# Kernel optimization log

Measured on AMD Instinct MI355X. Metric: run time of the kernel, lower is better.

Reference implementation:

```python
import jax, jax.numpy as jnp
import numpy as np

B, T, C = 4, 2048, 1024
H, D = 16, 64  # num_heads, head_size; H*D == C


def setup_inputs() -> dict:
    key = jax.random.key(0)
    ks = jax.random.split(key, 6)
    s = C ** -0.5
    return {
        "x": jax.random.normal(ks[0], (B, T, C), dtype=jnp.float32),
        "Wq": jax.random.normal(ks[1], (H, C, D), dtype=jnp.float32) * s,
        "Wk": jax.random.normal(ks[2], (H, C, D), dtype=jnp.float32) * s,
        "Wv": jax.random.normal(ks[3], (H, C, D), dtype=jnp.float32) * s,
        "Wo": jax.random.normal(ks[4], (C, C), dtype=jnp.float32) * s,
        "bo": jnp.zeros((C,), dtype=jnp.float32),
    }


def reference(x, Wq, Wk, Wv, Wo, bo):
    # Per-head projections, vectorized over heads: [B,T,C] x [H,C,D] -> [B,H,T,D]
    q = jnp.einsum("btc,hcd->bhtd", x, Wq)
    k = jnp.einsum("btc,hcd->bhtd", x, Wk)
    v = jnp.einsum("btc,hcd->bhtd", x, Wv)
    # NOTE: original scales by n_embd**-0.5 (input channel C), not head_size.
    scale = jnp.asarray(C, x.dtype) ** -0.5
    scores = jnp.einsum("bhtd,bhsd->bhts", q, k) * scale  # [B,H,T,T]
    causal = jnp.tril(jnp.ones((T, T), dtype=bool))
    scores = jnp.where(causal, scores, jnp.asarray(-jnp.inf, x.dtype))
    attn = jax.nn.softmax(scores, axis=-1)
    out = jnp.einsum("bhts,bhsd->bhtd", attn, v)  # [B,H,T,D]
    # concat heads: [B,T,H*D] == [B,T,C]
    out = out.transpose(0, 2, 1, 3).reshape(B, T, H * D)
    return out @ Wo.T + bo
```

## Files before the change

kernel.cpp:

```cpp
#include <hip/hip_runtime.h>
#include <hip/hip_bf16.h>
#include <math.h>

#define B_ 4
#define T_ 2048
#define C_ 1024
#define H_ 16
#define D_ 64
#define BT (B_*T_)
#define BH (B_*H_)

typedef __bf16 bf16x8 __attribute__((ext_vector_type(8)));
typedef __bf16 bf16x4 __attribute__((ext_vector_type(4)));
typedef float f32x4 __attribute__((ext_vector_type(4)));
typedef unsigned short u16;
typedef u16 u16x8 __attribute__((ext_vector_type(8)));

#define GLL(g, l) __builtin_amdgcn_global_load_lds( \
    (const __attribute__((address_space(1))) unsigned int*)(g), \
    (__attribute__((address_space(3))) unsigned int*)(l), 16, 0, 0)

#define SCALE2 0.04508422f

__device__ __forceinline__ u16 f2b(float f) {
    union { float f; unsigned u; } v; v.f = f;
    unsigned r = v.u + 0x7fffu + ((v.u >> 16) & 1u);
    return (u16)(r >> 16);
}

__global__ __launch_bounds__(256) void prep(const float* __restrict__ x,
                                            const float* __restrict__ Wo,
                                            const float* __restrict__ Wq,
                                            const float* __restrict__ Wk,
                                            const float* __restrict__ Wv,
                                            u16* __restrict__ xbf,
                                            u16* __restrict__ wobf,
                                            u16* __restrict__ wt) {
    __shared__ u16 lds[64][72];
    int bid = blockIdx.x, tid = threadIdx.x;
    if (bid < 8192) {
        int g = bid * 256 + tid;
        float4 v = ((const float4*)x)[g];
        ushort4 o;
        o.x = f2b(v.x); o.y = f2b(v.y); o.z = f2b(v.z); o.w = f2b(v.w);
        ((ushort4*)xbf)[g] = o;
        return;
    }
    if (bid < 9216) {
        int g = (bid - 8192) * 256 + tid;
        float4 v = ((const float4*)Wo)[g];
        ushort4 o;
        o.x = f2b(v.x); o.y = f2b(v.y); o.z = f2b(v.z); o.w = f2b(v.w);
        ((ushort4*)wobf)[g] = o;
        return;
    }
    int id = bid - 9216;
    int cb = id & 15, h = (id >> 4) & 15, w = id >> 8;
    const float* W = (w == 0) ? Wq : (w == 1) ? Wk : Wv;
    float sc = (w == 0) ? SCALE2 : 1.0f;
    int c0 = cb * 64;
    {
        int col = (tid & 15) * 4;
        for (int cc = 0; cc < 4; ++cc) {
            int r = (tid >> 4) + cc * 16;
            float4 v = *(const float4*)&W[(size_t)(h * C_ + c0 + r) * D_ + col];
            lds[r][col + 0] = f2b(v.x * sc); lds[r][col + 1] = f2b(v.y * sc);
            lds[r][col + 2] = f2b(v.z * sc); lds[r][col + 3] = f2b(v.w * sc);
        }
    }
    __syncthreads();
    {
        int tcol = (tid & 7) * 8;
        for (int cc = 0; cc < 2; ++cc) {
            int d = (tid >> 3) + cc * 32;
            u16x8 t;
            for (int j = 0; j < 8; ++j) t[j] = lds[tcol + j][d];
            *(u16x8*)&wt[(((size_t)(w * H_ + h) * D_ + d) * C_) + c0 + tcol] = t;
        }
    }
}

__global__ __launch_bounds__(256) void qkv_gemm(const u16* __restrict__ xbf,
                                                const u16* __restrict__ wt,
                                                u16* __restrict__ q, u16* __restrict__ k,
                                                u16* __restrict__ vt) {
    __shared__ u16 Al[128][64];
    __shared__ u16 Bl[128][64];
    int mb = blockIdx.x, nb = blockIdx.y;
    int tid = threadIdx.x, wv = tid >> 6, lane = tid & 63, l15 = lane & 15, quad = lane >> 4;
    int rowh = (wv & 1) * 64, colh = (wv >> 1) * 64;
    f32x4 acc[4][4];
    #pragma unroll
    for (int i = 0; i < 4; ++i)
        #pragma unroll
        for (int j = 0; j < 4; ++j) acc[i][j] = (f32x4){0.f, 0.f, 0.f, 0.f};
    int lrow = lane >> 3;
    int srow = wv * 32 + lrow;
    int scol = (((lane & 7) ^ lrow)) * 8;
    const u16* agp = &xbf[(size_t)(mb * 128 + srow) * C_ + scol];
    const u16* bgp = &wt[(size_t)(nb * 128 + srow) * C_ + scol];
    int rsw = l15 & 7;
    for (int k0 = 0; k0 < C_; k0 += 64) {
        #pragma unroll
        for (int j = 0; j < 4; ++j) {
            GLL(agp + (size_t)(j * 8) * C_ + k0, &Al[wv * 32 + j * 8][0]);
            GLL(bgp + (size_t)(j * 8) * C_ + k0, &Bl[wv * 32 + j * 8][0]);
        }
        __syncthreads();
        #pragma unroll
        for (int ks = 0; ks < 2; ++ks) {
            int cbl = (((ks << 2) | quad) ^ rsw) * 8;
            bf16x8 af[4], bf[4];
            #pragma unroll
            for (int mt = 0; mt < 4; ++mt)
                af[mt] = *(const bf16x8*)&Al[rowh + mt * 16 + l15][cbl];
            #pragma unroll
            for (int nt = 0; nt < 4; ++nt)
                bf[nt] = *(const bf16x8*)&Bl[colh + nt * 16 + l15][cbl];
            #pragma unroll
            for (int mt = 0; mt < 4; ++mt)
                #pragma unroll
                for (int nt = 0; nt < 4; ++nt)
                    acc[mt][nt] = __builtin_amdgcn_mfma_f32_16x16x32_bf16(af[mt], bf[nt], acc[mt][nt], 0, 0, 0);
        }
        __syncthreads();
    }
    int bb = (mb * 128) >> 11;
    #pragma unroll
    for (int nt = 0; nt < 4; ++nt) {
        int n0 = nb * 128 + colh + nt * 16;
        int wsel = n0 >> 10, hh = (n0 >> 6) & 15, d0 = n0 & 63;
        if (wsel == 2) {
            u16* vrow = vt + ((size_t)((bb * H_ + hh) * D_) + d0 + l15) * T_;
            #pragma unroll
            for (int mt = 0; mt < 4; ++mt) {
                int tbase = ((mb * 128 + rowh + mt * 16) & (T_ - 1)) + quad * 4;
                bf16x4 w;
                #pragma unroll
                for (int r = 0; r < 4; ++r) w[r] = (__bf16)acc[mt][nt][r];
                *(bf16x4*)&vrow[tbase] = w;
            }
        } else {
            u16* op = (wsel == 0) ? q : k;
            #pragma unroll
            for (int mt = 0; mt < 4; ++mt)
                #pragma unroll
                for (int r = 0; r < 4; ++r) {
                    int m = mb * 128 + rowh + mt * 16 + quad * 4 + r;
                    int tt = m & (T_ - 1);
                    op[((size_t)(bb * H_ + hh) * T_ + tt) * D_ + d0 + l15] = f2b(acc[mt][nt][r]);
                }
        }
    }
}

__global__ __launch_bounds__(256, 2) void attn(const u16* __restrict__ q, const u16* __restrict__ kk,
                                               const u16* __restrict__ vt, u16* __restrict__ att) {
    __shared__ u16 Kl[2][64][64];
    __shared__ u16 Vl[2][64][64];
    __shared__ u16 Pl[4][32][72];
    int bh = blockIdx.x, c = 15 - blockIdx.y;
    int b = bh >> 4, h = bh & 15;
    int tid = threadIdx.x, wid = tid >> 6, lane = tid & 63, l15 = lane & 15, quad = lane >> 4;
    const u16* qbase = q + (size_t)bh * T_ * D_;
    const u16* kbase = kk + (size_t)bh * T_ * D_;
    const u16* vbase = vt + (size_t)bh * D_ * T_;
    u16* pw = &Pl[wid][0][0];
    bf16x8 ones;
    #pragma unroll
    for (int j = 0; j < 8; ++j) ones[j] = (__bf16)1.0f;
    int r8 = lane >> 3, cbl_st = lane & 7;
    int csrc = ((cbl_st ^ r8)) * 8;
    int strow = wid * 16 + r8;
    int rsw = l15 & 7;

    int R0q = c * 128 + wid * 32;
    int ktb = 2 * c + 1;
    int kmax_w = R0q >> 6;
    bf16x8 bq[2][2];
    #pragma unroll
    for (int qt = 0; qt < 2; ++qt)
        #pragma unroll
        for (int kd = 0; kd < 2; ++kd)
            bq[qt][kd] = *(const bf16x8*)&qbase[(size_t)(R0q + qt * 16 + l15) * D_ + kd * 32 + quad * 8];
    f32x4 o[4][2];
    f32x4 lacc[2];
    #pragma unroll
    for (int dt = 0; dt < 4; ++dt)
        #pragma unroll
        for (int qt = 0; qt < 2; ++qt) o[dt][qt] = (f32x4){0.f, 0.f, 0.f, 0.f};
    lacc[0] = (f32x4){0.f, 0.f, 0.f, 0.f};
    lacc[1] = (f32x4){0.f, 0.f, 0.f, 0.f};
    #pragma unroll
    for (int j = 0; j < 2; ++j) {
        GLL(kbase + (size_t)(strow + j * 8) * D_ + csrc, &Kl[0][wid * 16 + j * 8][0]);
        GLL(vbase + (size_t)(strow + j * 8) * T_ + csrc, &Vl[0][wid * 16 + j * 8][0]);
    }
    __syncthreads();
    for (int kt = 0; kt <= ktb; ++kt) {
        int cur = kt & 1;
        if (kt < ktb) {
            int kn = (kt + 1) * 64;
            #pragma unroll
            for (int j = 0; j < 2; ++j) {
                GLL(kbase + (size_t)(kn + strow + j * 8) * D_ + csrc, &Kl[cur ^ 1][wid * 16 + j * 8][0]);
                GLL(vbase + (size_t)(strow + j * 8) * T_ + kn + csrc, &Vl[cur ^ 1][wid * 16 + j * 8][0]);
            }
        }
        if (kt <= kmax_w) {
            int k0 = kt * 64;
            f32x4 sS[4][2];
            #pragma unroll
            for (int kvt = 0; kvt < 4; ++kvt)
                #pragma unroll
                for (int qt = 0; qt < 2; ++qt) sS[kvt][qt] = (f32x4){0.f, 0.f, 0.f, 0.f};
            #pragma unroll
            for (int kd = 0; kd < 2; ++kd) {
                int cblk = (((kd << 2) | quad) ^ rsw) * 8;
                bf16x8 akf[4];
                #pragma unroll
                for (int kvt = 0; kvt < 4; ++kvt)
                    akf[kvt] = *(const bf16x8*)&Kl[cur][kvt * 16 + l15][cblk];
                #pragma unroll
                for (int kvt = 0; kvt < 4; ++kvt)
                    #pragma unroll
                    for (int qt = 0; qt < 2; ++qt)
                        sS[kvt][qt] = __builtin_amdgcn_mfma_f32_16x16x32_bf16(akf[kvt], bq[qt][kd], sS[kvt][qt], 0, 0, 0);
            }
            if (kt == kmax_w) {
                #pragma unroll
                for (int qt = 0; qt < 2; ++qt) {
                    int qabs = R0q + qt * 16 + l15;
                    #pragma unroll
                    for (int kvt = 0; kvt < 4; ++kvt) {
                        int kvb = k0 + kvt * 16 + quad * 4;
                        #pragma unroll
                        for (int r = 0; r < 4; ++r)
                            if (kvb + r > qabs) sS[kvt][qt][r] = -INFINITY;
                    }
                }
            }
            #pragma unroll
            for (int kvt = 0; kvt < 4; ++kvt)
                #pragma unroll
                for (int qt = 0; qt < 2; ++qt)
                    #pragma unroll
                    for (int r = 0; r < 4; ++r)
                        sS[kvt][qt][r] = __builtin_amdgcn_exp2f(sS[kvt][qt][r]);
            #pragma unroll
            for (int qt = 0; qt < 2; ++qt)
                #pragma unroll
                for (int kvt = 0; kvt < 4; ++kvt) {
                    bf16x4 w;
                    #pragma unroll
                    for (int r = 0; r < 4; ++r) w[r] = (__bf16)sS[kvt][qt][r];
                    *(bf16x4*)&pw[(qt * 16 + l15) * 72 + kvt * 16 + quad * 4] = w;
                }
            #pragma unroll
            for (int ks = 0; ks < 2; ++ks) {
                int cblk = (((ks << 2) | quad) ^ rsw) * 8;
                bf16x8 avf[4];
                #pragma unroll
                for (int dt = 0; dt < 4; ++dt)
                    avf[dt] = *(const bf16x8*)&Vl[cur][dt * 16 + l15][cblk];
                #pragma unroll
                for (int qt = 0; qt < 2; ++qt) {
                    bf16x8 bp = *(const bf16x8*)&pw[(qt * 16 + l15) * 72 + ks * 32 + quad * 8];
                    #pragma unroll
                    for (int dt = 0; dt < 4; ++dt)
                        o[dt][qt] = __builtin_amdgcn_mfma_f32_16x16x32_bf16(avf[dt], bp, o[dt][qt], 0, 0, 0);
                    lacc[qt] = __builtin_amdgcn_mfma_f32_16x16x32_bf16(ones, bp, lacc[qt], 0, 0, 0);
                }
            }
        }
        __syncthreads();
    }
    #pragma unroll
    for (int qt = 0; qt < 2; ++qt) {
        float rl = __builtin_amdgcn_rcpf(lacc[qt][0]);
        int qabs = R0q + qt * 16 + l15;
        #pragma unroll
        for (int dt = 0; dt < 4; ++dt) {
            bf16x4 w;
            #pragma unroll
            for (int r = 0; r < 4; ++r) w[r] = (__bf16)(o[dt][qt][r] * rl);
            *(bf16x4*)&att[(size_t)(b * T_ + qabs) * C_ + h * 64 + dt * 16 + quad * 4] = w;
        }
    }
}

__global__ __launch_bounds__(256) void out_gemm(const u16* __restrict__ att,
                                                const u16* __restrict__ wo,
                                                const float* __restrict__ bo,
                                                float* __restrict__ out) {
    __shared__ u16 Al[128][64];
    __shared__ u16 Bl[128][64];
    int mb = blockIdx.x, nb = blockIdx.y;
    int tid = threadIdx.x, wv = tid >> 6, lane = tid & 63, l15 = lane & 15, quad = lane >> 4;
    int rowh = (wv & 1) * 64, colh = (wv >> 1) * 64;
    f32x4 acc[4][4];
    #pragma unroll
    for (int i = 0; i < 4; ++i)
        #pragma unroll
        for (int j = 0; j < 4; ++j) acc[i][j] = (f32x4){0.f, 0.f, 0.f, 0.f};
    int lrow = lane >> 3;
    int srow = wv * 32 + lrow;
    int scol = (((lane & 7) ^ lrow)) * 8;
    const u16* agp = &att[(size_t)(mb * 128 + srow) * C_ + scol];
    const u16* bgp = &wo[(size_t)(nb * 128 + srow) * C_ + scol];
    int rsw = l15 & 7;
    for (int k0 = 0; k0 < C_; k0 += 64) {
        #pragma unroll
        for (int j = 0; j < 4; ++j) {
            GLL(agp + (size_t)(j * 8) * C_ + k0, &Al[wv * 32 + j * 8][0]);
            GLL(bgp + (size_t)(j * 8) * C_ + k0, &Bl[wv * 32 + j * 8][0]);
        }
        __syncthreads();
        #pragma unroll
        for (int ks = 0; ks < 2; ++ks) {
            int cbl = (((ks << 2) | quad) ^ rsw) * 8;
            bf16x8 af[4], bf[4];
            #pragma unroll
            for (int mt = 0; mt < 4; ++mt)
                af[mt] = *(const bf16x8*)&Al[rowh + mt * 16 + l15][cbl];
            #pragma unroll
            for (int nt = 0; nt < 4; ++nt)
                bf[nt] = *(const bf16x8*)&Bl[colh + nt * 16 + l15][cbl];
            #pragma unroll
            for (int mt = 0; mt < 4; ++mt)
                #pragma unroll
                for (int nt = 0; nt < 4; ++nt)
                    acc[mt][nt] = __builtin_amdgcn_mfma_f32_16x16x32_bf16(af[mt], bf[nt], acc[mt][nt], 0, 0, 0);
        }
        __syncthreads();
    }
    #pragma unroll
    for (int nt = 0; nt < 4; ++nt) {
        int n = nb * 128 + colh + nt * 16 + l15;
        float bias = bo[n];
        #pragma unroll
        for (int mt = 0; mt < 4; ++mt)
            #pragma unroll
            for (int r = 0; r < 4; ++r) {
                int m = mb * 128 + rowh + mt * 16 + quad * 4 + r;
                out[(size_t)m * C_ + n] = acc[mt][nt][r] + bias;
            }
    }
}

extern "C" void kernel_launch(void* const* d_in, const int* in_sizes, int n_in,
                              void* d_out, int out_size, void* d_ws, size_t ws_size,
                              hipStream_t stream) {
    const float* x  = (const float*)d_in[0];
    const float* Wq = (const float*)d_in[1];
    const float* Wk = (const float*)d_in[2];
    const float* Wv = (const float*)d_in[3];
    const float* Wo = (const float*)d_in[4];
    const float* bo = (const float*)d_in[5];
    float* out = (float*)d_out;
    char* ws = (char*)d_ws;
    u16* xbf  = (u16*)(ws + (size_t)0);
    u16* wt   = (u16*)(ws + ((size_t)16 << 20));
    u16* wobf = (u16*)(ws + ((size_t)22 << 20));
    u16* qb   = (u16*)(ws + ((size_t)24 << 20));
    u16* kb   = (u16*)(ws + ((size_t)40 << 20));
    u16* vtb  = (u16*)(ws + ((size_t)56 << 20));
    u16* attb = (u16*)(ws + ((size_t)72 << 20));

    hipLaunchKernelGGL(prep, dim3(9984), dim3(256), 0, stream, x, Wo, Wq, Wk, Wv, xbf, wobf, wt);
    hipLaunchKernelGGL(qkv_gemm, dim3(BT / 128, 3 * C_ / 128), dim3(256), 0, stream, xbf, wt, qb, kb, vtb);
    hipLaunchKernelGGL(attn, dim3(BH, 16), dim3(256), 0, stream, qb, kb, vtb, attb);
    hipLaunchKernelGGL(out_gemm, dim3(BT / 128, C_ / 128), dim3(256), 0, stream, attb, wobf, bo, out);
}
```

Baseline: 227.3 us.

## Restructure QKV GEMM with 256x192 tiles, double-buffered LDS, and interleaved prefetch

The QKV projection GEMM moves from 128x128 tiles with 4 waves and a load-sync-compute loop to 256x192 tiles with 8 waves per 512-thread block. LDS is double buffered, and global-to-LDS loads for the next k-tile are interleaved into four MFMA phases using manual vmcnt/lgkmcnt waits, barriers and setprio. A 1D grid with an XCD-aware block remap replaces the 2D grid, which should improve L2 locality across chiplets. The aim is to hide memory latency and raise arithmetic intensity. In exchange it adds many barriers, a more fragile hand-written sync schedule and higher register pressure.

```diff
diff --git a/kernel.cpp b/kernel.cpp
--- a/kernel.cpp
+++ b/kernel.cpp
@@ -21,6 +21,10 @@
     (__attribute__((address_space(3))) unsigned int*)(l), 16, 0, 0)
 
 #define SCALE2 0.04508422f
+
+#define SBAR()   do { asm volatile("" ::: "memory"); __builtin_amdgcn_s_barrier(); asm volatile("" ::: "memory"); } while (0)
+#define WAITV(n) asm volatile("s_waitcnt vmcnt(" #n ")" ::: "memory")
+#define LGKM0()  asm volatile("s_waitcnt lgkmcnt(0)" ::: "memory")
 
 __device__ __forceinline__ u16 f2b(float f) {
     union { float f; unsigned u; } v; v.f = f;
@@ -80,75 +84,115 @@
     }
 }
 
-__global__ __launch_bounds__(256) void qkv_gemm(const u16* __restrict__ xbf,
-                                                const u16* __restrict__ wt,
-                                                u16* __restrict__ q, u16* __restrict__ k,
-                                                u16* __restrict__ vt) {
-    __shared__ u16 Al[128][64];
-    __shared__ u16 Bl[128][64];
-    int mb = blockIdx.x, nb = blockIdx.y;
-    int tid = threadIdx.x, wv = tid >> 6, lane = tid & 63, l15 = lane & 15, quad = lane >> 4;
-    int rowh = (wv & 1) * 64, colh = (wv >> 1) * 64;
-    f32x4 acc[4][4];
-    #pragma unroll
-    for (int i = 0; i < 4; ++i)
-        #pragma unroll
-        for (int j = 0; j < 4; ++j) acc[i][j] = (f32x4){0.f, 0.f, 0.f, 0.f};
-    int lrow = lane >> 3;
-    int srow = wv * 32 + lrow;
-    int scol = (((lane & 7) ^ lrow)) * 8;
-    const u16* agp = &xbf[(size_t)(mb * 128 + srow) * C_ + scol];
-    const u16* bgp = &wt[(size_t)(nb * 128 + srow) * C_ + scol];
+#define NT_ 16
+__global__ __launch_bounds__(512, 2) void qkv_gemm(const u16* __restrict__ xbf,
+                                                   const u16* __restrict__ wt,
+                                                   u16* __restrict__ q, u16* __restrict__ k,
+                                                   u16* __restrict__ vt) {
+    __shared__ u16 Al[2][256][64];
+    __shared__ u16 Bl[2][192][64];
+    int orig = blockIdx.x;
+    int wg = (orig & 7) * 64 + (orig >> 3);
+    int mb = wg & 31, nb = wg >> 5;
+    int tid = threadIdx.x, wid = tid >> 6, lane = tid & 63;
+    int l15 = lane & 15, quad = lane >> 4;
+    int wm = wid >> 2, wn = wid & 3;
+    int srow8 = wid * 8 + (lane >> 3);
+    int scol8 = ((lane & 7) ^ (lane >> 3)) * 8;
+    const u16* Ag = xbf + (size_t)(mb * 256 + srow8) * C_ + scol8;
+    const u16* Bg = wt  + (size_t)(nb * 192 + srow8) * C_ + scol8;
     int rsw = l15 & 7;
-    for (int k0 = 0; k0 < C_; k0 += 64) {
-        #pragma unroll
-        for (int j = 0; j < 4; ++j) {
-            GLL(agp + (size_t)(j * 8) * C_ + k0, &Al[wv * 32 + j * 8][0]);
-            GLL(bgp + (size_t)(j * 8) * C_ + k0, &Bl[wv * 32 + j * 8][0]);
-        }
-        __syncthreads();
-        #pragma unroll
-        for (int ks = 0; ks < 2; ++ks) {
-            int cbl = (((ks << 2) | quad) ^ rsw) * 8;
-            bf16x8 af[4], bf[4];
-            #pragma unroll
-            for (int mt = 0; mt < 4; ++mt)
-                af[mt] = *(const bf16x8*)&Al[rowh + mt * 16 + l15][cbl];
-            #pragma unroll
-            for (int nt = 0; nt < 4; ++nt)
-                bf[nt] = *(const bf16x8*)&Bl[colh + nt * 16 + l15][cbl];
-            #pragma unroll
-            for (int mt = 0; mt < 4; ++mt)
-                #pragma unroll
-                for (int nt = 0; nt < 4; ++nt)
-                    acc[mt][nt] = __builtin_amdgcn_mfma_f32_16x16x32_bf16(af[mt], bf[nt], acc[mt][nt], 0, 0, 0);
-        }
-        __syncthreads();
-    }
-    int bb = (mb * 128) >> 11;
-    #pragma unroll
-    for (int nt = 0; nt < 4; ++nt) {
-        int n0 = nb * 128 + colh + nt * 16;
+    f32x4 acc[8][3];
+    #pragma unroll
+    for (int i = 0; i < 8; ++i)
+        #pragma unroll
+        for (int j = 0; j < 3; ++j) acc[i][j] = (f32x4){0.f, 0.f, 0.f, 0.f};
+
+#define STAGE_A(buf, u, kt) GLL(Ag + (size_t)((u) * 64) * C_ + (kt) * 64, &Al[buf][(u) * 64 + wid * 8][0])
+#define STAGE_B(buf, u, kt) GLL(Bg + (size_t)((u) * 64) * C_ + (kt) * 64, &Bl[buf][(u) * 64 + wid * 8][0])
+#define LOAD_A(R0) do { \
+    _Pragma("unroll") for (int r = 0; r < 2; ++r) \
+    _Pragma("unroll") for (int ks = 0; ks < 2; ++ks) \
+        a[r][ks] = *(const bf16x8*)&Ac[wm * 128 + ((R0) + r) * 16 + l15][(((ks << 2) | quad) ^ rsw) * 8]; \
+} while (0)
+#define MFMA_PH(R0) do { \
+    __builtin_amdgcn_s_setprio(1); \
+    _Pragma("unroll") for (int ks = 0; ks < 2; ++ks) \
+    _Pragma("unroll") for (int fc = 0; fc < 3; ++fc) \
+    _Pragma("unroll") for (int r = 0; r < 2; ++r) \
+        acc[(R0) + r][fc] = __builtin_amdgcn_mfma_f32_16x16x32_bf16(a[r][ks], b[fc][ks], acc[(R0) + r][fc], 0, 0, 0); \
+    __builtin_amdgcn_s_setprio(0); \
+} while (0)
+
+    STAGE_A(0, 0, 0); STAGE_A(0, 1, 0); STAGE_A(0, 2, 0); STAGE_A(0, 3, 0);
+    STAGE_B(0, 0, 0); STAGE_B(0, 1, 0); STAGE_B(0, 2, 0);
+    STAGE_B(1, 0, 1); STAGE_B(1, 1, 1); STAGE_B(1, 2, 1);
+    WAITV(3);
+    SBAR();
+
+    for (int t = 0; t < NT_; ++t) {
+        int cur = t & 1, nxt = cur ^ 1;
+        const u16 (*Ac)[64] = Al[cur];
+        const u16 (*Bc)[64] = Bl[cur];
+        bf16x8 b[3][2], a[2][2];
+        #pragma unroll
+        for (int fc = 0; fc < 3; ++fc)
+            #pragma unroll
+            for (int ks = 0; ks < 2; ++ks)
+                b[fc][ks] = *(const bf16x8*)&Bc[wn * 48 + fc * 16 + l15][(((ks << 2) | quad) ^ rsw) * 8];
+        LOAD_A(0);
+        if (t + 1 < NT_) { STAGE_A(nxt, 0, t + 1); STAGE_A(nxt, 1, t + 1); }
+        SBAR(); LGKM0();
+        MFMA_PH(0);
+        SBAR();
+        LOAD_A(2);
+        if (t + 1 < NT_) { STAGE_A(nxt, 2, t + 1); STAGE_A(nxt, 3, t + 1); }
+        SBAR(); LGKM0();
+        MFMA_PH(2);
+        SBAR();
+        LOAD_A(4);
+        if (t + 2 < NT_) { STAGE_B(cur, 0, t + 2); STAGE_B(cur, 1, t + 2); }
+        SBAR(); LGKM0();
+        MFMA_PH(4);
+        SBAR();
+        LOAD_A(6);
+        if (t + 2 < NT_) STAGE_B(cur, 2, t + 2);
+        SBAR(); LGKM0();
+        MFMA_PH(6);
+        if (t + 2 < NT_)      WAITV(3);
+        else if (t + 1 < NT_) WAITV(0);
+        SBAR();
+    }
+#undef STAGE_A
+#undef STAGE_B
+#undef LOAD_A
+#undef MFMA_PH
+
+    int bb = mb >> 3;
+    int mbase0 = mb * 256 + wm * 128;
+    #pragma unroll
+    for (int fc = 0; fc < 3; ++fc) {
+        int n0 = nb * 192 + wn * 48 + fc * 16;
         int wsel = n0 >> 10, hh = (n0 >> 6) & 15, d0 = n0 & 63;
         if (wsel == 2) {
             u16* vrow = vt + ((size_t)((bb * H_ + hh) * D_) + d0 + l15) * T_;
             #pragma unroll
-            for (int mt = 0; mt < 4; ++mt) {
-                int tbase = ((mb * 128 + rowh + mt * 16) & (T_ - 1)) + quad * 4;
+            for (int fr = 0; fr < 8; ++fr) {
+                int tbase = ((mbase0 + fr * 16) & (T_ - 1)) + quad * 4;
                 bf16x4 w;
                 #pragma unroll
-                for (int r = 0; r < 4; ++r) w[r] = (__bf16)acc[mt][nt][r];
+                for (int r = 0; r < 4; ++r) w[r] = (__bf16)acc[fr][fc][r];
                 *(bf16x4*)&vrow[tbase] = w;
             }
         } else {
-            u16* op = (wsel == 0) ? q : k;
-            #pragma unroll
-            for (int mt = 0; mt < 4; ++mt)
+            u16* op = wsel ? k : q;
+            #pragma unroll
+            for (int fr = 0; fr < 8; ++fr)
                 #pragma unroll
                 for (int r = 0; r < 4; ++r) {
-                    int m = mb * 128 + rowh + mt * 16 + quad * 4 + r;
+                    int m = mbase0 + fr * 16 + quad * 4 + r;
                     int tt = m & (T_ - 1);
-                    op[((size_t)(bb * H_ + hh) * T_ + tt) * D_ + d0 + l15] = f2b(acc[mt][nt][r]);
+                    op[((size_t)(bb * H_ + hh) * T_ + tt) * D_ + d0 + l15] = f2b(acc[fr][fc][r]);
                 }
         }
     }
@@ -368,7 +412,7 @@
     u16* attb = (u16*)(ws + ((size_t)72 << 20));
 
     hipLaunchKernelGGL(prep, dim3(9984), dim3(256), 0, stream, x, Wo, Wq, Wk, Wv, xbf, wobf, wt);
-    hipLaunchKernelGGL(qkv_gemm, dim3(BT / 128, 3 * C_ / 128), dim3(256), 0, stream, xbf, wt, qb, kb, vtb);
+    hipLaunchKernelGGL(qkv_gemm, dim3(512), dim3(512), 0, stream, xbf, wt, qb, kb, vtb);
     hipLaunchKernelGGL(attn, dim3(BH, 16), dim3(256), 0, stream, qb, kb, vtb, attb);
     hipLaunchKernelGGL(out_gemm, dim3(BT / 128, C_ / 128), dim3(256), 0, stream, attb, wobf, bo, out);
 }
```

Result: slower. 241.1 us (+6.1%).
